# Optimization experiments

Hardware: AMD Instinct MI355X
Metric: run time of the kernel (lower is better)

The kernel has to match this reference:

```python
import jax, jax.numpy as jnp
import numpy as np

N_EMBD = 1024
N_HEAD = 16
HEAD_DIM = N_EMBD // N_HEAD
B, T = 2, 2048


def setup_inputs() -> dict:
    key = jax.random.key(0)
    ks = jax.random.split(key, 9)
    s = 1.0 / np.sqrt(N_EMBD)
    return {
        "x": jax.random.normal(ks[0], (B, T, N_EMBD), dtype=jnp.float32),
        "Wq": jax.random.normal(ks[1], (N_EMBD, N_EMBD), dtype=jnp.float32) * s,
        "bq": jax.random.normal(ks[2], (N_EMBD,), dtype=jnp.float32) * s,
        "Wk": jax.random.normal(ks[3], (N_EMBD, N_EMBD), dtype=jnp.float32) * s,
        "bk": jax.random.normal(ks[4], (N_EMBD,), dtype=jnp.float32) * s,
        "Wv": jax.random.normal(ks[5], (N_EMBD, N_EMBD), dtype=jnp.float32) * s,
        "bv": jax.random.normal(ks[6], (N_EMBD,), dtype=jnp.float32) * s,
        "Wp": jax.random.normal(ks[7], (N_EMBD, N_EMBD), dtype=jnp.float32) * s,
        "bp": jax.random.normal(ks[8], (N_EMBD,), dtype=jnp.float32) * s,
    }


def reference(x, Wq, bq, Wk, bk, Wv, bv, Wp, bp):
    b, t, c = x.shape
    # torch Linear: y = x @ W.T + b
    def proj(W, bias):
        y = jnp.einsum('btc,oc->bto', x, W) + bias
        return y.reshape(b, t, N_HEAD, HEAD_DIM).transpose(0, 2, 1, 3)  # [B,H,T,D]

    q = proj(Wq, bq)
    k = proj(Wk, bk)
    v = proj(Wv, bv)

    scale = 1.0 / np.sqrt(HEAD_DIM).astype(np.float32)
    scores = jnp.einsum('bhqd,bhkd->bhqk', q, k) * scale  # [B,H,T,T]
    causal = jnp.tril(jnp.ones((t, t), dtype=bool))
    scores = jnp.where(causal[None, None], scores, jnp.float32(-jnp.inf))
    attn = jax.nn.softmax(scores, axis=-1)
    out = jnp.einsum('bhqk,bhkd->bhqd', attn, v)  # [B,H,T,D]
    out = out.transpose(0, 2, 1, 3).reshape(b, t, c)
    out = jnp.einsum('btc,oc->bto', out, Wp) + bp
    return out
```

## Files before the change

### kernel.cpp

```cpp
#include <hip/hip_runtime.h>
#include <hip/hip_bf16.h>

#define TT 2048
#define MM 4096

typedef __attribute__((ext_vector_type(8))) short bf16x8;
typedef __attribute__((ext_vector_type(4))) float f32x4;

__device__ inline short f2bf(float f){
  union { float f; unsigned u; } x; x.f = f;
  unsigned r = x.u + 0x7FFFu + ((x.u >> 16) & 1u);
  return (short)(r >> 16);
}
__device__ inline int pk2bf(float a, float b){
  __hip_bfloat162 h2 = __float22bfloat162_rn(make_float2(a, b));
  return *(int*)&h2;
}

__device__ inline void async16(const void* g, void* l){
  __builtin_amdgcn_global_load_lds((const __attribute__((address_space(1))) void*)g,
                                   (__attribute__((address_space(3))) void*)l, 16, 0, 0);
}

__global__ void cvt_all(const float* __restrict__ x,
                        const float* __restrict__ Wq, const float* __restrict__ Wk,
                        const float* __restrict__ Wv, const float* __restrict__ Wp,
                        short* __restrict__ xb, short* __restrict__ Wqb, short* __restrict__ Wkb,
                        short* __restrict__ Wvb, short* __restrict__ Wpb){
  int b = blockIdx.x;
  const float* in; short* out; int base;
  if (b < 4096)      { in = x;  out = xb;  base = b; }
  else if (b < 5120) { in = Wq; out = Wqb; base = b - 4096; }
  else if (b < 6144) { in = Wk; out = Wkb; base = b - 5120; }
  else if (b < 7168) { in = Wv; out = Wvb; base = b - 6144; }
  else               { in = Wp; out = Wpb; base = b - 7168; }
  int i = base * 256 + threadIdx.x;
  float4 v = ((const float4*)in)[i];
  short4 o;
  o.x = f2bf(v.x); o.y = f2bf(v.y); o.z = f2bf(v.z); o.w = f2bf(v.w);
  ((short4*)out)[i] = o;
}

__device__ inline void gemm_core(const short* __restrict__ A, const short* __restrict__ Wm,
                                 short* As, short* Bs, int m0, int n0,
                                 int tid, int wm, int wn, int quad, int lr,
                                 f32x4 acc[4][4])
{
  const int prow = tid >> 2, pcol = (tid & 3) << 3;
  const short* Ap0 = A  + (size_t)(m0 + prow) * 1024 + pcol;
  const short* Ap1 = A  + (size_t)(m0 + prow + 64) * 1024 + pcol;
  const short* Bp0 = Wm + (size_t)(n0 + prow) * 1024 + pcol;
  const short* Bp1 = Wm + (size_t)(n0 + prow + 64) * 1024 + pcol;
  for (int kt = 0; kt < 16; ++kt){
    const int kk = kt * 64;
#pragma unroll
    for (int pn = 0; pn < 2; ++pn){
      async16(Ap0 + kk + pn*32, As + pn*4096 + (size_t)tid * 8);
      async16(Ap1 + kk + pn*32, As + pn*4096 + (size_t)(tid + 256) * 8);
      async16(Bp0 + kk + pn*32, Bs + pn*4096 + (size_t)tid * 8);
      async16(Bp1 + kk + pn*32, Bs + pn*4096 + (size_t)(tid + 256) * 8);
    }
    __syncthreads();
#pragma unroll
    for (int ks = 0; ks < 2; ++ks){
      bf16x8 aF[4], bF[4];
#pragma unroll
      for (int mt = 0; mt < 4; ++mt) aF[mt] = *(const bf16x8*)(As + ks*4096 + (wm*64 + mt*16 + lr)*32 + quad*8);
#pragma unroll
      for (int nt = 0; nt < 4; ++nt) bF[nt] = *(const bf16x8*)(Bs + ks*4096 + (wn*64 + nt*16 + lr)*32 + quad*8);
#pragma unroll
      for (int mt = 0; mt < 4; ++mt)
#pragma unroll
        for (int nt = 0; nt < 4; ++nt)
          acc[mt][nt] = __builtin_amdgcn_mfma_f32_16x16x32_bf16(aF[mt], bF[nt], acc[mt][nt], 0, 0, 0);
    }
    __syncthreads();
  }
}

__launch_bounds__(256, 3)
__global__ void gemm_qkv(const short* __restrict__ A,
                         const short* __restrict__ W0, const short* __restrict__ W1, const short* __restrict__ W2,
                         const float* __restrict__ b0, const float* __restrict__ b1, const float* __restrict__ b2,
                         short* __restrict__ Qo, short* __restrict__ Ko, short* __restrict__ Vt)
{
  __shared__ __align__(16) short smem[16384];
  short* As = smem;
  short* Bs = smem + 8192;
  const int z = blockIdx.z;
  const short* Wm   = (z == 0) ? W0 : ((z == 1) ? W1 : W2);
  const float* bias = (z == 0) ? b0 : ((z == 1) ? b1 : b2);
  const int tid = threadIdx.x;
  const int lane = tid & 63, wave = tid >> 6;
  const int wm = wave >> 1, wn = wave & 1;
  const int quad = lane >> 4, lr = lane & 15;
  const int m0 = blockIdx.y * 128, n0 = blockIdx.x * 128;

  f32x4 acc[4][4];
#pragma unroll
  for (int i = 0; i < 4; ++i)
#pragma unroll
    for (int j = 0; j < 4; ++j)
#pragma unroll
      for (int r = 0; r < 4; ++r) acc[i][j][r] = 0.f;

  gemm_core(A, Wm, As, Bs, m0, n0, tid, wm, wn, quad, lr, acc);

  const float qscale = 0.125f * 1.4426950408889634f;
  const int bB = m0 >> 11, t0 = m0 & 2047;

  if (z == 2){
#pragma unroll
    for (int nh = 0; nh < 2; ++nh){
      __syncthreads();
      if (wn == nh){
#pragma unroll
        for (int nt = 0; nt < 4; ++nt){
          int n = n0 + wn*64 + nt*16 + lr;
          float bv = bias[n];
          int n_l = nt*16 + lr;
#pragma unroll
          for (int mt = 0; mt < 4; ++mt)
#pragma unroll
            for (int r = 0; r < 4; ++r){
              int m_l = wm*64 + mt*16 + quad*4 + r;
              smem[n_l*136 + m_l] = f2bf(acc[mt][nt][r] + bv);
            }
        }
      }
      __syncthreads();
#pragma unroll
      for (int i = 0; i < 4; ++i){
        int c = tid + i*256;
        int rowN = c >> 4, ch = c & 15;
        int4 v = *(const int4*)(smem + rowN*136 + ch*8);
        int n = n0 + nh*64 + rowN;
        int hH = n >> 6, d = n & 63;
        *(int4*)(Vt + ((size_t)((bB<<4) + hH)*64 + d)*2048 + t0 + ch*8) = v;
      }
    }
    return;
  }

  short* dst = (z == 0) ? Qo : Ko;
#pragma unroll
  for (int nh = 0; nh < 2; ++nh){
    __syncthreads();
    if (wn == nh){
#pragma unroll
      for (int nt = 0; nt < 4; ++nt){
        int n_l = nt*16 + lr;
        float bv = bias[n0 + nh*64 + n_l];
#pragma unroll
        for (int mt = 0; mt < 4; ++mt){
#pragma unroll
          for (int r = 0; r < 4; ++r){
            int m_l = wm*64 + mt*16 + quad*4 + r;
            float v = acc[mt][nt][r] + bv;
            if (z == 0) v *= qscale;
            smem[m_l*72 + n_l] = f2bf(v);
          }
        }
      }
    }
    __syncthreads();
    const int hH = (n0 + nh*64) >> 6;
    short* dhead = dst + (size_t)((bB<<4) + hH) * 2048 * 64;
#pragma unroll
    for (int i = 0; i < 4; ++i){
      int c = tid + i*256;
      int rowm = c >> 3, ch = (c & 7) << 3;
      int4 v = *(const int4*)(smem + rowm*72 + ch);
      *(int4*)(dhead + (size_t)(t0 + rowm)*64 + ch) = v;
    }
  }
}

__launch_bounds__(256, 2)
__global__ void gemm_proj(const short* __restrict__ A, const short* __restrict__ Wm,
                          const float* __restrict__ bias, float* __restrict__ out)
{
  __shared__ __align__(16) short As[2*4096];
  __shared__ __align__(16) short Bs[2*2048];
  const int tid = threadIdx.x;
  const int lane = tid & 63, wave = tid >> 6;
  const int quad = lane >> 4, lr = lane & 15;
  const int m0 = blockIdx.y * 128, n0 = blockIdx.x * 64;

  const int prow = tid >> 2, pcol = (tid & 3) << 3;
  const short* Ap0 = A  + (size_t)(m0 + prow) * 1024 + pcol;
  const short* Ap1 = A  + (size_t)(m0 + prow + 64) * 1024 + pcol;
  const short* Bp0 = Wm + (size_t)(n0 + (tid >> 2)) * 1024 + pcol;

  f32x4 acc[2][4];
#pragma unroll
  for (int i = 0; i < 2; ++i)
#pragma unroll
    for (int j = 0; j < 4; ++j)
#pragma unroll
      for (int r = 0; r < 4; ++r) acc[i][j][r] = 0.f;

  for (int kt = 0; kt < 16; ++kt){
    const int kk = kt * 64;
#pragma unroll
    for (int pn = 0; pn < 2; ++pn){
      async16(Ap0 + kk + pn*32, As + pn*4096 + (size_t)tid * 8);
      async16(Ap1 + kk + pn*32, As + pn*4096 + (size_t)(tid + 256) * 8);
      async16(Bp0 + kk + pn*32, Bs + pn*2048 + (size_t)tid * 8);
    }
    __syncthreads();
#pragma unroll
    for (int ks = 0; ks < 2; ++ks){
      bf16x8 aF[2], bF[4];
#pragma unroll
      for (int mt = 0; mt < 2; ++mt) aF[mt] = *(const bf16x8*)(As + ks*4096 + (wave*32 + mt*16 + lr)*32 + quad*8);
#pragma unroll
      for (int nt = 0; nt < 4; ++nt) bF[nt] = *(const bf16x8*)(Bs + ks*2048 + (nt*16 + lr)*32 + quad*8);
#pragma unroll
      for (int mt = 0; mt < 2; ++mt)
#pragma unroll
        for (int nt = 0; nt < 4; ++nt)
          acc[mt][nt] = __builtin_amdgcn_mfma_f32_16x16x32_bf16(aF[mt], bF[nt], acc[mt][nt], 0, 0, 0);
    }
    __syncthreads();
  }

#pragma unroll
  for (int nt = 0; nt < 4; ++nt){
    int n = n0 + nt*16 + lr;
    float bv = bias[n];
#pragma unroll
    for (int mt = 0; mt < 2; ++mt){
      int mBase = m0 + wave*32 + mt*16 + quad*4;
#pragma unroll
      for (int r = 0; r < 4; ++r){
        int m = mBase + r;
        out[(size_t)m * 1024 + n] = acc[mt][nt][r] + bv;
      }
    }
  }
}

__launch_bounds__(256, 4)
__global__ void attn_kernel(const short* __restrict__ Q, const short* __restrict__ K,
                            const short* __restrict__ Vt, short* __restrict__ AO)
{
  __shared__ __align__(16) short Ks[2][4096];
  __shared__ __align__(16) short Vs[2][4096];
  __shared__ __align__(16) short Ps[4096];
  const int tid = threadIdx.x, lane = tid & 63, wave = tid >> 6;
  const int quad = lane >> 4, lr = lane & 15;
  const int bid = blockIdx.x;
  const int chunk = bid >> 8;
  const int a = (bid >> 5) & 7;
  int qt;
  if      (chunk == 0) qt = 31 - a;
  else if (chunk == 1) qt = a;
  else if (chunk == 2) qt = 23 - a;
  else                 qt = 8 + a;
  const int hb = bid & 31;
  const int bidx = hb >> 4, h = hb & 15;
  const int q0 = qt * 64;
  const int wq = q0 + wave * 16;
  const short* Qh = Q  + (size_t)hb * TT * 64;
  const short* Kh = K  + (size_t)hb * TT * 64;
  const short* Vh = Vt + (size_t)hb * 64 * TT;
  short* Pw = Ps + wave * 1024;

  const int srow = tid >> 3;
  const int ssw  = (tid & 7) ^ (srow & 7);
  const short* Kp0 = Kh + (size_t)srow * 64 + ssw * 8;
  const short* Vp0 = Vh + (size_t)srow * TT + ssw * 8;

  bf16x8 qf[2];
#pragma unroll
  for (int ks = 0; ks < 2; ++ks)
    qf[ks] = *(const bf16x8*)(Qh + (size_t)(wq + lr) * 64 + ks*32 + quad*8);

  const int lsw0 = (((0*4 + quad) ^ (lr & 7)) << 3);
  const int lsw1 = (((1*4 + quad) ^ (lr & 7)) << 3);
  const int qh2 = quad >> 1, qlo = (quad & 1) << 2;

  f32x4 acc_o[4], l_acc;
#pragma unroll
  for (int r = 0; r < 4; ++r) l_acc[r] = 0.f;
#pragma unroll
  for (int dt = 0; dt < 4; ++dt)
#pragma unroll
    for (int r = 0; r < 4; ++r) acc_o[dt][r] = 0.f;

  const short one_bf = (short)0x3F80;
  const bf16x8 onesf = { one_bf, one_bf, one_bf, one_bf, one_bf, one_bf, one_bf, one_bf };

  const int nkv = qt + 1;
  async16(Kp0,           &Ks[0][(size_t)tid * 8]);
  async16(Kp0 + 32*64,   &Ks[0][(size_t)(tid + 256) * 8]);
  async16(Vp0,           &Vs[0][(size_t)tid * 8]);
  async16(Vp0 + 32*TT,   &Vs[0][(size_t)(tid + 256) * 8]);

  int cur = 0;
  for (int kv = 0; kv < nkv; ++kv){
    const int kv0 = kv * 64;
    __syncthreads();
    if (kv + 1 < nkv){
      const short* kp = Kp0 + (size_t)(kv + 1) * 4096;
      const short* vp = Vp0 + (kv + 1) * 64;
      const int nb = cur ^ 1;
      async16(kp,          &Ks[nb][(size_t)tid * 8]);
      async16(kp + 32*64,  &Ks[nb][(size_t)(tid + 256) * 8]);
      async16(vp,          &Vs[nb][(size_t)tid * 8]);
      async16(vp + 32*TT,  &Vs[nb][(size_t)(tid + 256) * 8]);
    }
    if (kv0 <= wq + 15){
      f32x4 s4[4];
#pragma unroll
      for (int nt = 0; nt < 4; ++nt)
#pragma unroll
        for (int r = 0; r < 4; ++r) s4[nt][r] = 0.f;
#pragma unroll
      for (int nt = 0; nt < 4; ++nt){
        bf16x8 kf0 = *(const bf16x8*)(&Ks[cur][(nt*16 + lr)*64 + lsw0]);
        bf16x8 kf1 = *(const bf16x8*)(&Ks[cur][(nt*16 + lr)*64 + lsw1]);
        s4[nt] = __builtin_amdgcn_mfma_f32_16x16x32_bf16(kf0, qf[0], s4[nt], 0, 0, 0);
        s4[nt] = __builtin_amdgcn_mfma_f32_16x16x32_bf16(kf1, qf[1], s4[nt], 0, 0, 0);
      }

      const bool need_mask = (kv == nkv - 1);
      const int qglob = wq + lr;
#pragma unroll
      for (int nt = 0; nt < 4; ++nt){
        const int keyb = kv0 + nt*16 + quad*4;
        float pv[4];
#pragma unroll
        for (int r = 0; r < 4; ++r){
          float v = exp2f(s4[nt][r]);
          if (need_mask && keyb + r > qglob) v = 0.f;
          pv[r] = v;
        }
        int2 w;
        w.x = pk2bf(pv[0], pv[1]);
        w.y = pk2bf(pv[2], pv[3]);
        const int g = nt*2 + qh2;
        *(int2*)(Pw + lr*64 + ((g ^ (lr & 7)) << 3) + qlo) = w;
      }

#pragma unroll
      for (int ks = 0; ks < 2; ++ks){
        const int lsw = ks ? lsw1 : lsw0;
        bf16x8 ptf = *(const bf16x8*)(Pw + lr*64 + lsw);
        l_acc = __builtin_amdgcn_mfma_f32_16x16x32_bf16(onesf, ptf, l_acc, 0, 0, 0);
#pragma unroll
        for (int dt = 0; dt < 4; ++dt){
          bf16x8 vf = *(const bf16x8*)(&Vs[cur][(dt*16 + lr)*64 + lsw]);
          acc_o[dt] = __builtin_amdgcn_mfma_f32_16x16x32_bf16(vf, ptf, acc_o[dt], 0, 0, 0);
        }
      }
    }
    cur ^= 1;
  }

  const float inv = __builtin_amdgcn_rcpf(l_acc[0]);
#pragma unroll
  for (int dt = 0; dt < 4; ++dt){
    int2 w;
    w.x = pk2bf(acc_o[dt][0] * inv, acc_o[dt][1] * inv);
    w.y = pk2bf(acc_o[dt][2] * inv, acc_o[dt][3] * inv);
    const int g = dt*2 + qh2;
    *(int2*)(Pw + lr*64 + ((g ^ (lr & 7)) << 3) + qlo) = w;
  }
#pragma unroll
  for (int i = 0; i < 2; ++i){
    int c = lane + i*64;
    int row = c >> 3, ch = c & 7;
    int4 v = *(const int4*)(Pw + row*64 + ((ch ^ (row & 7)) << 3));
    *(int4*)(AO + (size_t)(bidx*2048 + wq + row)*1024 + h*64 + ch*8) = v;
  }
}

extern "C" void kernel_launch(void* const* d_in, const int* in_sizes, int n_in,
                              void* d_out, int out_size, void* d_ws, size_t ws_size,
                              hipStream_t stream)
{
  const float* x  = (const float*)d_in[0];
  const float* Wq = (const float*)d_in[1];
  const float* bq = (const float*)d_in[2];
  const float* Wk = (const float*)d_in[3];
  const float* bk = (const float*)d_in[4];
  const float* Wv = (const float*)d_in[5];
  const float* bv = (const float*)d_in[6];
  const float* Wp = (const float*)d_in[7];
  const float* bp = (const float*)d_in[8];
  float* out = (float*)d_out;

  char* ws = (char*)d_ws;
  const size_t MB = 1024ull * 1024ull;
  short* Qb  = (short*)(ws + 0);
  short* Kb  = (short*)(ws + 8*MB);
  short* Vtb = (short*)(ws + 16*MB);
  short* AOb = (short*)(ws + 24*MB);
  short* xb  = (short*)(ws + 24*MB);
  short* Wqb = (short*)(ws + 32*MB);
  short* Wkb = (short*)(ws + 34*MB);
  short* Wvb = (short*)(ws + 36*MB);
  short* Wpb = (short*)(ws + 38*MB);

  cvt_all<<<8192, 256, 0, stream>>>(x, Wq, Wk, Wv, Wp, xb, Wqb, Wkb, Wvb, Wpb);
  gemm_qkv<<<dim3(8, 32, 3), 256, 0, stream>>>(xb, Wqb, Wkb, Wvb, bq, bk, bv, Qb, Kb, Vtb);
  attn_kernel<<<1024, 256, 0, stream>>>(Qb, Kb, Vtb, AOb);
  gemm_proj<<<dim3(16, 32), 256, 0, stream>>>(AOb, Wpb, bp, out);
}
```

Baseline: 178.9 us.

## Split long causal attention tiles across two blocks with a combine kernel

Query tiles 16-31 now have their KV range split into two halves, each processed by a separate block. The blocks write unnormalized fp32 partial outputs and row sums to workspace, and a new combine kernel adds the halves, normalizes and writes bf16. A constant task table sets the scheduling order and the KV ranges, and blocks with long KV ranges raise their wave priority. The aim is better load balance and shorter tail latency for causal attention, at the cost of extra fp32 traffic and one more kernel launch. Summing the two halves without a max is valid because the softmax uses no max subtraction, so the partials share a scale.

```diff
diff --git a/kernel.cpp b/kernel.cpp
--- a/kernel.cpp
+++ b/kernel.cpp
@@ -241,9 +241,23 @@
   }
 }
 
+__device__ __constant__ int task_tbl[48] = {
+  31760, 32272, 30736, 15376,
+  31247, 29711, 30191, 28687, 14351,
+  29166, 27662, 28110, 26638, 13326,
+  27085, 25613, 26029, 24589, 12301,
+  25004, 23564, 23948, 22540, 11276,
+  22923, 21515, 21867, 20491, 10251,
+  20842, 19466, 19786, 18442,  9226,
+  18761, 17417, 17705, 16393,  8201,
+  16680,  7176,
+   6151,  5126,  4101,  3076,  2051,  1026, 1
+};
+
 __launch_bounds__(256, 4)
 __global__ void attn_kernel(const short* __restrict__ Q, const short* __restrict__ K,
-                            const short* __restrict__ Vt, short* __restrict__ AO)
+                            const short* __restrict__ Vt, short* __restrict__ AO,
+                            float* __restrict__ Opart, float* __restrict__ Lpart)
 {
   __shared__ __align__(16) short Ks[2][4096];
   __shared__ __align__(16) short Vs[2][4096];
@@ -251,14 +265,11 @@
   const int tid = threadIdx.x, lane = tid & 63, wave = tid >> 6;
   const int quad = lane >> 4, lr = lane & 15;
   const int bid = blockIdx.x;
-  const int chunk = bid >> 8;
-  const int a = (bid >> 5) & 7;
-  int qt;
-  if      (chunk == 0) qt = 31 - a;
-  else if (chunk == 1) qt = a;
-  else if (chunk == 2) qt = 23 - a;
-  else                 qt = 8 + a;
+  const int e  = task_tbl[bid >> 5];
+  const int qt = e >> 10, kv_s = (e >> 5) & 31, kvn = e & 31;
   const int hb = bid & 31;
+  const bool split = (qt >= 16);
+  const int half = (kv_s != 0) ? 1 : 0;
   const int bidx = hb >> 4, h = hb & 15;
   const int q0 = qt * 64;
   const int wq = q0 + wave * 16;
@@ -267,6 +278,8 @@
   const short* Vh = Vt + (size_t)hb * 64 * TT;
   short* Pw = Ps + wave * 1024;
 
+  if (kvn >= 14) __builtin_amdgcn_s_setprio(1);
+
   const int srow = tid >> 3;
   const int ssw  = (tid & 7) ^ (srow & 7);
   const short* Kp0 = Kh + (size_t)srow * 64 + ssw * 8;
@@ -292,17 +305,21 @@
   const short one_bf = (short)0x3F80;
   const bf16x8 onesf = { one_bf, one_bf, one_bf, one_bf, one_bf, one_bf, one_bf, one_bf };
 
-  const int nkv = qt + 1;
-  async16(Kp0,           &Ks[0][(size_t)tid * 8]);
-  async16(Kp0 + 32*64,   &Ks[0][(size_t)(tid + 256) * 8]);
-  async16(Vp0,           &Vs[0][(size_t)tid * 8]);
-  async16(Vp0 + 32*TT,   &Vs[0][(size_t)(tid + 256) * 8]);
+  const int kv_e = kv_s + kvn;
+  {
+    const short* kp = Kp0 + (size_t)kv_s * 4096;
+    const short* vp = Vp0 + kv_s * 64;
+    async16(kp,          &Ks[0][(size_t)tid * 8]);
+    async16(kp + 32*64,  &Ks[0][(size_t)(tid + 256) * 8]);
+    async16(vp,          &Vs[0][(size_t)tid * 8]);
+    async16(vp + 32*TT,  &Vs[0][(size_t)(tid + 256) * 8]);
+  }
 
   int cur = 0;
-  for (int kv = 0; kv < nkv; ++kv){
+  for (int kv = kv_s; kv < kv_e; ++kv){
     const int kv0 = kv * 64;
     __syncthreads();
-    if (kv + 1 < nkv){
+    if (kv + 1 < kv_e){
       const short* kp = Kp0 + (size_t)(kv + 1) * 4096;
       const short* vp = Vp0 + (kv + 1) * 64;
       const int nb = cur ^ 1;
@@ -311,7 +328,7 @@
       async16(vp,          &Vs[nb][(size_t)tid * 8]);
       async16(vp + 32*TT,  &Vs[nb][(size_t)(tid + 256) * 8]);
     }
-    if (kv0 <= wq + 15){
+    {
       f32x4 s4[4];
 #pragma unroll
       for (int nt = 0; nt < 4; ++nt)
@@ -325,7 +342,7 @@
         s4[nt] = __builtin_amdgcn_mfma_f32_16x16x32_bf16(kf1, qf[1], s4[nt], 0, 0, 0);
       }
 
-      const bool need_mask = (kv == nkv - 1);
+      const bool need_mask = (kv == qt);
       const int qglob = wq + lr;
 #pragma unroll
       for (int nt = 0; nt < 4; ++nt){
@@ -359,6 +376,17 @@
     cur ^= 1;
   }
 
+  if (split){
+    const int p = (((hb << 4) | (qt - 16)) << 1) + half;
+    float* Op = Opart + (size_t)p * 4096;
+    const int q_l = wave*16 + lr;
+#pragma unroll
+    for (int dt = 0; dt < 4; ++dt)
+      *(f32x4*)(Op + q_l*64 + dt*16 + quad*4) = acc_o[dt];
+    if (lane < 16) Lpart[p*64 + wave*16 + lane] = l_acc[0];
+    return;
+  }
+
   const float inv = __builtin_amdgcn_rcpf(l_acc[0]);
 #pragma unroll
   for (int dt = 0; dt < 4; ++dt){
@@ -375,6 +403,25 @@
     int4 v = *(const int4*)(Pw + row*64 + ((ch ^ (row & 7)) << 3));
     *(int4*)(AO + (size_t)(bidx*2048 + wq + row)*1024 + h*64 + ch*8) = v;
   }
+}
+
+__global__ void attn_combine(const float* __restrict__ Opart, const float* __restrict__ Lpart,
+                             short* __restrict__ AO)
+{
+  const int gid = blockIdx.x * 256 + threadIdx.x;
+  const int row = gid >> 4, dq = (gid & 15) << 2;
+  const int hb = row >> 10, qt16 = (row >> 6) & 15, r = row & 63;
+  const int p = ((hb << 4) | qt16) << 1;
+  const f32x4 a = *(const f32x4*)(Opart + (size_t)p*4096 + r*64 + dq);
+  const f32x4 b = *(const f32x4*)(Opart + (size_t)(p+1)*4096 + r*64 + dq);
+  const float l = Lpart[p*64 + r] + Lpart[(p+1)*64 + r];
+  const float inv = __builtin_amdgcn_rcpf(l);
+  int2 w;
+  w.x = pk2bf((a[0]+b[0])*inv, (a[1]+b[1])*inv);
+  w.y = pk2bf((a[2]+b[2])*inv, (a[3]+b[3])*inv);
+  const int t = (16 + qt16)*64 + r;
+  const int bidx = hb >> 4, h = hb & 15;
+  *(int2*)(AO + (size_t)(bidx*2048 + t)*1024 + h*64 + dq) = w;
 }
 
 extern "C" void kernel_launch(void* const* d_in, const int* in_sizes, int n_in,
@@ -403,9 +450,12 @@
   short* Wkb = (short*)(ws + 34*MB);
   short* Wvb = (short*)(ws + 36*MB);
   short* Wpb = (short*)(ws + 38*MB);
+  float* Opart = (float*)(ws + 40*MB);
+  float* Lpart = (float*)(ws + 56*MB);
 
   cvt_all<<<8192, 256, 0, stream>>>(x, Wq, Wk, Wv, Wp, xb, Wqb, Wkb, Wvb, Wpb);
   gemm_qkv<<<dim3(8, 32, 3), 256, 0, stream>>>(xb, Wqb, Wkb, Wvb, bq, bk, bv, Qb, Kb, Vtb);
-  attn_kernel<<<1024, 256, 0, stream>>>(Qb, Kb, Vtb, AOb);
+  attn_kernel<<<1536, 256, 0, stream>>>(Qb, Kb, Vtb, AOb, Opart, Lpart);
+  attn_combine<<<2048, 256, 0, stream>>>(Opart, Lpart, AOb);
   gemm_proj<<<dim3(16, 32), 256, 0, stream>>>(AOb, Wpb, bp, out);
 }
```

Measured after the change: 187.8 us. +5.0%, slower.

## Process 128 queries per attention block to reuse K/V tiles across two query groups

Applied to the files above, without the earlier changes.

Each attention block now handles 128 query rows, so each wave covers 32 rows as two 16-row groups. Every K/V tile loaded into shared memory is used by twice as many MFMAs, which halves the K/V global traffic and async-load work per query. The grid is halved to 512 blocks with a simpler two-pass heavy/light ordering. In exchange, register and LDS use rise (launch bounds drop to 2 blocks per SIMD, P buffer doubled), there are fewer blocks to balance the causal workload, and the diagonal blocks do more masked work.

```diff
diff --git a/kernel.cpp b/kernel.cpp
--- a/kernel.cpp
+++ b/kernel.cpp
@@ -241,58 +241,59 @@
   }
 }
 
-__launch_bounds__(256, 4)
+__launch_bounds__(256, 2)
 __global__ void attn_kernel(const short* __restrict__ Q, const short* __restrict__ K,
                             const short* __restrict__ Vt, short* __restrict__ AO)
 {
   __shared__ __align__(16) short Ks[2][4096];
   __shared__ __align__(16) short Vs[2][4096];
-  __shared__ __align__(16) short Ps[4096];
+  __shared__ __align__(16) short Ps[8192];
   const int tid = threadIdx.x, lane = tid & 63, wave = tid >> 6;
   const int quad = lane >> 4, lr = lane & 15;
   const int bid = blockIdx.x;
-  const int chunk = bid >> 8;
+  const int pass = bid >> 8;
   const int a = (bid >> 5) & 7;
-  int qt;
-  if      (chunk == 0) qt = 31 - a;
-  else if (chunk == 1) qt = a;
-  else if (chunk == 2) qt = 23 - a;
-  else                 qt = 8 + a;
   const int hb = bid & 31;
+  const int qb = pass ? a : (15 - a);
   const int bidx = hb >> 4, h = hb & 15;
-  const int q0 = qt * 64;
-  const int wq = q0 + wave * 16;
+  const int wq0 = qb * 128 + wave * 32;
   const short* Qh = Q  + (size_t)hb * TT * 64;
   const short* Kh = K  + (size_t)hb * TT * 64;
   const short* Vh = Vt + (size_t)hb * 64 * TT;
-  short* Pw = Ps + wave * 1024;
+  short* Pw = Ps + wave * 2048;
 
   const int srow = tid >> 3;
   const int ssw  = (tid & 7) ^ (srow & 7);
   const short* Kp0 = Kh + (size_t)srow * 64 + ssw * 8;
   const short* Vp0 = Vh + (size_t)srow * TT + ssw * 8;
 
-  bf16x8 qf[2];
-#pragma unroll
-  for (int ks = 0; ks < 2; ++ks)
-    qf[ks] = *(const bf16x8*)(Qh + (size_t)(wq + lr) * 64 + ks*32 + quad*8);
+  bf16x8 qf[2][2];
+#pragma unroll
+  for (int g = 0; g < 2; ++g)
+#pragma unroll
+    for (int ks = 0; ks < 2; ++ks)
+      qf[g][ks] = *(const bf16x8*)(Qh + (size_t)(wq0 + g*16 + lr) * 64 + ks*32 + quad*8);
 
   const int lsw0 = (((0*4 + quad) ^ (lr & 7)) << 3);
   const int lsw1 = (((1*4 + quad) ^ (lr & 7)) << 3);
   const int qh2 = quad >> 1, qlo = (quad & 1) << 2;
 
-  f32x4 acc_o[4], l_acc;
-#pragma unroll
-  for (int r = 0; r < 4; ++r) l_acc[r] = 0.f;
-#pragma unroll
-  for (int dt = 0; dt < 4; ++dt)
-#pragma unroll
-    for (int r = 0; r < 4; ++r) acc_o[dt][r] = 0.f;
+  f32x4 acc_o[2][4], l_acc[2];
+#pragma unroll
+  for (int g = 0; g < 2; ++g){
+#pragma unroll
+    for (int r = 0; r < 4; ++r) l_acc[g][r] = 0.f;
+#pragma unroll
+    for (int dt = 0; dt < 4; ++dt)
+#pragma unroll
+      for (int r = 0; r < 4; ++r) acc_o[g][dt][r] = 0.f;
+  }
 
   const short one_bf = (short)0x3F80;
   const bf16x8 onesf = { one_bf, one_bf, one_bf, one_bf, one_bf, one_bf, one_bf, one_bf };
 
-  const int nkv = qt + 1;
+  const int nkv = 2*qb + 2;
+  const int qtw = wq0 >> 6;
   async16(Kp0,           &Ks[0][(size_t)tid * 8]);
   async16(Kp0 + 32*64,   &Ks[0][(size_t)(tid + 256) * 8]);
   async16(Vp0,           &Vs[0][(size_t)tid * 8]);
@@ -311,69 +312,85 @@
       async16(vp,          &Vs[nb][(size_t)tid * 8]);
       async16(vp + 32*TT,  &Vs[nb][(size_t)(tid + 256) * 8]);
     }
-    if (kv0 <= wq + 15){
-      f32x4 s4[4];
-#pragma unroll
-      for (int nt = 0; nt < 4; ++nt)
-#pragma unroll
-        for (int r = 0; r < 4; ++r) s4[nt][r] = 0.f;
+    if (kv0 <= wq0 + 31){
+      f32x4 s4[2][4];
+#pragma unroll
+      for (int g = 0; g < 2; ++g)
+#pragma unroll
+        for (int nt = 0; nt < 4; ++nt)
+#pragma unroll
+          for (int r = 0; r < 4; ++r) s4[g][nt][r] = 0.f;
 #pragma unroll
       for (int nt = 0; nt < 4; ++nt){
         bf16x8 kf0 = *(const bf16x8*)(&Ks[cur][(nt*16 + lr)*64 + lsw0]);
         bf16x8 kf1 = *(const bf16x8*)(&Ks[cur][(nt*16 + lr)*64 + lsw1]);
-        s4[nt] = __builtin_amdgcn_mfma_f32_16x16x32_bf16(kf0, qf[0], s4[nt], 0, 0, 0);
-        s4[nt] = __builtin_amdgcn_mfma_f32_16x16x32_bf16(kf1, qf[1], s4[nt], 0, 0, 0);
-      }
-
-      const bool need_mask = (kv == nkv - 1);
-      const int qglob = wq + lr;
-#pragma unroll
-      for (int nt = 0; nt < 4; ++nt){
-        const int keyb = kv0 + nt*16 + quad*4;
-        float pv[4];
-#pragma unroll
-        for (int r = 0; r < 4; ++r){
-          float v = exp2f(s4[nt][r]);
-          if (need_mask && keyb + r > qglob) v = 0.f;
-          pv[r] = v;
+#pragma unroll
+        for (int g = 0; g < 2; ++g){
+          s4[g][nt] = __builtin_amdgcn_mfma_f32_16x16x32_bf16(kf0, qf[g][0], s4[g][nt], 0, 0, 0);
+          s4[g][nt] = __builtin_amdgcn_mfma_f32_16x16x32_bf16(kf1, qf[g][1], s4[g][nt], 0, 0, 0);
         }
-        int2 w;
-        w.x = pk2bf(pv[0], pv[1]);
-        w.y = pk2bf(pv[2], pv[3]);
-        const int g = nt*2 + qh2;
-        *(int2*)(Pw + lr*64 + ((g ^ (lr & 7)) << 3) + qlo) = w;
+      }
+
+      const bool need_mask = (kv == qtw);
+#pragma unroll
+      for (int g = 0; g < 2; ++g){
+        const int qglob = wq0 + g*16 + lr;
+        short* Pg = Pw + g*1024;
+#pragma unroll
+        for (int nt = 0; nt < 4; ++nt){
+          const int keyb = kv0 + nt*16 + quad*4;
+          float pv[4];
+#pragma unroll
+          for (int r = 0; r < 4; ++r){
+            float v = exp2f(s4[g][nt][r]);
+            if (need_mask && keyb + r > qglob) v = 0.f;
+            pv[r] = v;
+          }
+          int2 w;
+          w.x = pk2bf(pv[0], pv[1]);
+          w.y = pk2bf(pv[2], pv[3]);
+          const int gg = nt*2 + qh2;
+          *(int2*)(Pg + lr*64 + ((gg ^ (lr & 7)) << 3) + qlo) = w;
+        }
       }
 
 #pragma unroll
       for (int ks = 0; ks < 2; ++ks){
         const int lsw = ks ? lsw1 : lsw0;
-        bf16x8 ptf = *(const bf16x8*)(Pw + lr*64 + lsw);
-        l_acc = __builtin_amdgcn_mfma_f32_16x16x32_bf16(onesf, ptf, l_acc, 0, 0, 0);
+        bf16x8 ptf0 = *(const bf16x8*)(Pw + lr*64 + lsw);
+        bf16x8 ptf1 = *(const bf16x8*)(Pw + 1024 + lr*64 + lsw);
+        l_acc[0] = __builtin_amdgcn_mfma_f32_16x16x32_bf16(onesf, ptf0, l_acc[0], 0, 0, 0);
+        l_acc[1] = __builtin_amdgcn_mfma_f32_16x16x32_bf16(onesf, ptf1, l_acc[1], 0, 0, 0);
 #pragma unroll
         for (int dt = 0; dt < 4; ++dt){
           bf16x8 vf = *(const bf16x8*)(&Vs[cur][(dt*16 + lr)*64 + lsw]);
-          acc_o[dt] = __builtin_amdgcn_mfma_f32_16x16x32_bf16(vf, ptf, acc_o[dt], 0, 0, 0);
+          acc_o[0][dt] = __builtin_amdgcn_mfma_f32_16x16x32_bf16(vf, ptf0, acc_o[0][dt], 0, 0, 0);
+          acc_o[1][dt] = __builtin_amdgcn_mfma_f32_16x16x32_bf16(vf, ptf1, acc_o[1][dt], 0, 0, 0);
         }
       }
     }
     cur ^= 1;
   }
 
-  const float inv = __builtin_amdgcn_rcpf(l_acc[0]);
-#pragma unroll
-  for (int dt = 0; dt < 4; ++dt){
-    int2 w;
-    w.x = pk2bf(acc_o[dt][0] * inv, acc_o[dt][1] * inv);
-    w.y = pk2bf(acc_o[dt][2] * inv, acc_o[dt][3] * inv);
-    const int g = dt*2 + qh2;
-    *(int2*)(Pw + lr*64 + ((g ^ (lr & 7)) << 3) + qlo) = w;
-  }
-#pragma unroll
-  for (int i = 0; i < 2; ++i){
-    int c = lane + i*64;
-    int row = c >> 3, ch = c & 7;
-    int4 v = *(const int4*)(Pw + row*64 + ((ch ^ (row & 7)) << 3));
-    *(int4*)(AO + (size_t)(bidx*2048 + wq + row)*1024 + h*64 + ch*8) = v;
+#pragma unroll
+  for (int g = 0; g < 2; ++g){
+    short* Pg = Pw + g*1024;
+    const float inv = __builtin_amdgcn_rcpf(l_acc[g][0]);
+#pragma unroll
+    for (int dt = 0; dt < 4; ++dt){
+      int2 w;
+      w.x = pk2bf(acc_o[g][dt][0] * inv, acc_o[g][dt][1] * inv);
+      w.y = pk2bf(acc_o[g][dt][2] * inv, acc_o[g][dt][3] * inv);
+      const int gg = dt*2 + qh2;
+      *(int2*)(Pg + lr*64 + ((gg ^ (lr & 7)) << 3) + qlo) = w;
+    }
+#pragma unroll
+    for (int i = 0; i < 2; ++i){
+      int c = lane + i*64;
+      int row = c >> 3, ch = c & 7;
+      int4 v = *(const int4*)(Pg + row*64 + ((ch ^ (row & 7)) << 3));
+      *(int4*)(AO + (size_t)(bidx*2048 + wq0 + g*16 + row)*1024 + h*64 + ch*8) = v;
+    }
   }
 }
 
@@ -406,6 +423,6 @@
 
   cvt_all<<<8192, 256, 0, stream>>>(x, Wq, Wk, Wv, Wp, xb, Wqb, Wkb, Wvb, Wpb);
   gemm_qkv<<<dim3(8, 32, 3), 256, 0, stream>>>(xb, Wqb, Wkb, Wvb, bq, bk, bv, Qb, Kb, Vtb);
-  attn_kernel<<<1024, 256, 0, stream>>>(Qb, Kb, Vtb, AOb);
+  attn_kernel<<<512, 256, 0, stream>>>(Qb, Kb, Vtb, AOb);
   gemm_proj<<<dim3(16, 32), 256, 0, stream>>>(AOb, Wpb, bp, out);
 }
```

New measurement: 197.2 us. +10.2%, slower.
